# Optimization experiments

Hardware: AMD Instinct MI355X
Metric: run time of the kernel (lower is better)

## Reference

```python
import jax, jax.numpy as jnp
import numpy as np

N_G, E_G, E_H, E_I = 100000, 1000000, 1500000, 2000000
IN_FEATS = 64


def setup_inputs() -> dict:
    key = jax.random.key(0)
    ks = jax.random.split(key, 13)
    inp = {
        'z': jax.random.randint(ks[0], (N_G,), 0, 8),
        'src_g': jax.random.randint(ks[1], (E_G,), 0, N_G),
        'dst_g': jax.random.randint(ks[2], (E_G,), 0, N_G),
        'src_h': jax.random.randint(ks[3], (E_H,), 0, E_G),
        'dst_h': jax.random.randint(ks[4], (E_H,), 0, E_G),
        'src_i': jax.random.randint(ks[5], (E_I,), 0, E_H),
        'dst_i': jax.random.randint(ks[6], (E_I,), 0, E_H),
    }
    for n, k in zip(['e1', 'e2', 'e3', 'e4', 'e5', 'e6'], ks[7:13]):
        inp[n] = jax.random.normal(k, (2, IN_FEATS), dtype=jnp.float32)
    return inp


def reference(z, src_g, dst_g, src_h, dst_h, src_i, dst_i, e1, e2, e3, e4, e5, e6):
    # hop 1: g.apply_edges(send_z) -> per-edge endpoint labels, become h node data
    z_src = z[src_g]            # [E_G]
    z_dst = z[dst_g]            # [E_G]
    # hop 2: h.apply_edges(send_z2) -> become i node data
    z_src_src = z_src[src_h]    # [E_H]
    z_dst_dst = z_dst[dst_h]    # [E_H]
    # hop 3: i.apply_edges(comparison4) on edge endpoints of i
    za = z_src_src[src_i]       # [E_I]
    zb = z_src_src[dst_i]
    zc = z_dst_dst[src_i]
    zd = z_dst_dst[dst_i]
    zac = (za == zc).astype(jnp.int32)
    zab = (za == zb).astype(jnp.int32)
    zbc = (zc == zb).astype(jnp.int32)
    zad = (za == zd).astype(jnp.int32)
    zcd = (zc == zd).astype(jnp.int32)
    zbd = (zb == zd).astype(jnp.int32)
    # six 2-row embedding lookups summed -> [E_I, IN_FEATS]
    h = e1[zac] + e2[zab] + e3[zbc] + e4[zad] + e5[zcd] + e6[zbd]
    return h
```

## Files before the change

kernel.cpp:

```cpp
#include <hip/hip_runtime.h>


#define N_FEAT 64
#define WEPB   4096

typedef float f4 __attribute__((ext_vector_type(4)));

__global__ void hop1_table_kernel(const int* __restrict__ z,
                                  const int* __restrict__ src_g,
                                  const int* __restrict__ dst_g,
                                  unsigned short* __restrict__ zg,
                                  const float* __restrict__ e1,
                                  const float* __restrict__ e2,
                                  const float* __restrict__ e3,
                                  const float* __restrict__ e4,
                                  const float* __restrict__ e5,
                                  const float* __restrict__ e6,
                                  float* __restrict__ table,
                                  int n) {
    int i  = blockIdx.x * blockDim.x + threadIdx.x;
    int n8 = n >> 3;
    if (i < n8) {
        const int4* s4 = (const int4*)src_g;
        const int4* d4 = (const int4*)dst_g;
        int4 sa = s4[2 * i], sb = s4[2 * i + 1];
        int4 da = d4[2 * i], db = d4[2 * i + 1];
        unsigned r0 = ((unsigned)z[sa.x] & 0xffu) | (((unsigned)z[da.x] & 0xffu) << 8)
                    | (((unsigned)z[sa.y] & 0xffu) << 16) | (((unsigned)z[da.y] & 0xffu) << 24);
        unsigned r1 = ((unsigned)z[sa.z] & 0xffu) | (((unsigned)z[da.z] & 0xffu) << 8)
                    | (((unsigned)z[sa.w] & 0xffu) << 16) | (((unsigned)z[da.w] & 0xffu) << 24);
        unsigned r2 = ((unsigned)z[sb.x] & 0xffu) | (((unsigned)z[db.x] & 0xffu) << 8)
                    | (((unsigned)z[sb.y] & 0xffu) << 16) | (((unsigned)z[db.y] & 0xffu) << 24);
        unsigned r3 = ((unsigned)z[sb.z] & 0xffu) | (((unsigned)z[db.z] & 0xffu) << 8)
                    | (((unsigned)z[sb.w] & 0xffu) << 16) | (((unsigned)z[db.w] & 0xffu) << 24);
        ((uint4*)zg)[i] = make_uint4(r0, r1, r2, r3);
    } else {
        int e = (n8 << 3) + (i - n8);
        if (e < n) {
            zg[e] = (unsigned short)(((unsigned)z[src_g[e]] & 0xffu)
                                   | (((unsigned)z[dst_g[e]] & 0xffu) << 8));
        }
    }
    if (blockIdx.x < 16) {
        int idx = blockIdx.x * 256 + threadIdx.x;
        int cmb = idx >> 6;
        int f   = idx & (N_FEAT - 1);
        float v = e1[((cmb >> 0) & 1) * N_FEAT + f];
        v      += e2[((cmb >> 1) & 1) * N_FEAT + f];
        v      += e3[((cmb >> 2) & 1) * N_FEAT + f];
        v      += e4[((cmb >> 3) & 1) * N_FEAT + f];
        v      += e5[((cmb >> 4) & 1) * N_FEAT + f];
        v      += e6[((cmb >> 5) & 1) * N_FEAT + f];
        table[idx] = v;
    }
}

__global__ void hop2_kernel(const unsigned short* __restrict__ zg,
                            const int* __restrict__ src_h,
                            const int* __restrict__ dst_h,
                            unsigned short* __restrict__ zh,
                            int n) {
    int i  = blockIdx.x * blockDim.x + threadIdx.x;
    int n8 = n >> 3;
    if (i < n8) {
        const int4* s4 = (const int4*)src_h;
        const int4* d4 = (const int4*)dst_h;
        int4 sa = s4[2 * i], sb = s4[2 * i + 1];
        int4 da = d4[2 * i], db = d4[2 * i + 1];
        unsigned a0 = zg[sa.x], b0 = zg[da.x];
        unsigned a1 = zg[sa.y], b1 = zg[da.y];
        unsigned a2 = zg[sa.z], b2 = zg[da.z];
        unsigned a3 = zg[sa.w], b3 = zg[da.w];
        unsigned a4 = zg[sb.x], b4 = zg[db.x];
        unsigned a5 = zg[sb.y], b5 = zg[db.y];
        unsigned a6 = zg[sb.z], b6 = zg[db.z];
        unsigned a7 = zg[sb.w], b7 = zg[db.w];
        unsigned r0 = (a0 & 0xffu) | (b0 & 0xff00u) | ((a1 & 0xffu) << 16) | ((b1 & 0xff00u) << 16);
        unsigned r1 = (a2 & 0xffu) | (b2 & 0xff00u) | ((a3 & 0xffu) << 16) | ((b3 & 0xff00u) << 16);
        unsigned r2 = (a4 & 0xffu) | (b4 & 0xff00u) | ((a5 & 0xffu) << 16) | ((b5 & 0xff00u) << 16);
        unsigned r3 = (a6 & 0xffu) | (b6 & 0xff00u) | ((a7 & 0xffu) << 16) | ((b7 & 0xff00u) << 16);
        ((uint4*)zh)[i] = make_uint4(r0, r1, r2, r3);
    } else {
        int e = (n8 << 3) + (i - n8);
        if (e < n) {
            unsigned a = zg[src_h[e]], b = zg[dst_h[e]];
            zh[e] = (unsigned short)((a & 0xffu) | (b & 0xff00u));
        }
    }
}

__device__ __forceinline__ unsigned combo6(unsigned p, unsigned q) {
    unsigned za = p & 0xffu, zc = p >> 8;
    unsigned zb = q & 0xffu, zd = q >> 8;
    return (unsigned)(za == zc)
         | ((unsigned)(za == zb) << 1)
         | ((unsigned)(zc == zb) << 2)
         | ((unsigned)(za == zd) << 3)
         | ((unsigned)(zc == zd) << 4)
         | ((unsigned)(zb == zd) << 5);
}

__global__ __launch_bounds__(256)
void fused_k3_kernel(const unsigned short* __restrict__ zh,
                     const int* __restrict__ src_i,
                     const int* __restrict__ dst_i,
                     const float* __restrict__ table,
                     float* __restrict__ out,
                     int nEdges) {
    __shared__ f4   tbl[64 * 16];
    __shared__ uint4 cmbv[WEPB / 16];
    const int tid = threadIdx.x;
    const long long e0 = (long long)blockIdx.x * WEPB;
    int nb = nEdges - (int)e0; if (nb > WEPB) nb = WEPB;

    const f4* t4 = (const f4*)table;
#pragma unroll
    for (int k = 0; k < 4; ++k)
        tbl[k * 256 + tid] = t4[k * 256 + tid];

    if (nb == WEPB) {
        const int4* si = (const int4*)(src_i + e0);
        const int4* di = (const int4*)(dst_i + e0);
        int4 s0 = si[tid * 4 + 0], s1 = si[tid * 4 + 1],
             s2 = si[tid * 4 + 2], s3 = si[tid * 4 + 3];
        int4 d0 = di[tid * 4 + 0], d1 = di[tid * 4 + 1],
             d2 = di[tid * 4 + 2], d3 = di[tid * 4 + 3];
        unsigned r0 =  combo6(zh[s0.x], zh[d0.x])
                    | (combo6(zh[s0.y], zh[d0.y]) << 8)
                    | (combo6(zh[s0.z], zh[d0.z]) << 16)
                    | (combo6(zh[s0.w], zh[d0.w]) << 24);
        unsigned r1 =  combo6(zh[s1.x], zh[d1.x])
                    | (combo6(zh[s1.y], zh[d1.y]) << 8)
                    | (combo6(zh[s1.z], zh[d1.z]) << 16)
                    | (combo6(zh[s1.w], zh[d1.w]) << 24);
        unsigned r2 =  combo6(zh[s2.x], zh[d2.x])
                    | (combo6(zh[s2.y], zh[d2.y]) << 8)
                    | (combo6(zh[s2.z], zh[d2.z]) << 16)
                    | (combo6(zh[s2.w], zh[d2.w]) << 24);
        unsigned r3 =  combo6(zh[s3.x], zh[d3.x])
                    | (combo6(zh[s3.y], zh[d3.y]) << 8)
                    | (combo6(zh[s3.z], zh[d3.z]) << 16)
                    | (combo6(zh[s3.w], zh[d3.w]) << 24);
        cmbv[tid] = make_uint4(r0, r1, r2, r3);
    } else {
        unsigned r[4] = {0u, 0u, 0u, 0u};
        for (int j = 0; j < 16; ++j) {
            int le = tid * 16 + j;
            if (le < nb) {
                long long e = e0 + le;
                unsigned c = combo6(zh[src_i[e]], zh[dst_i[e]]);
                r[j >> 2] |= c << ((j & 3) * 8);
            }
        }
        cmbv[tid] = make_uint4(r[0], r[1], r[2], r[3]);
    }
    __syncthreads();

    const unsigned char* cmb = (const unsigned char*)cmbv;
    const int  w      = tid >> 6;
    const int  lane   = tid & 63;
    const int  c      = lane & 15;
    const int  leBase = w * (WEPB / 4) + (lane >> 4);
    const long long fBase = e0 * 16 + (long long)w * (WEPB * 16 / 4) + lane;
    constexpr int ITER = WEPB * 16 / 4 / 64;

    if (nb == WEPB) {
#pragma unroll 4
        for (int i = 0; i < ITER; ++i) {
            int le = leBase + i * 4;
            ((f4*)out)[fBase + (long long)i * 64] = tbl[(int)cmb[le] * 16 + c];
        }
    } else {
        const long long total = (long long)nEdges * 16;
#pragma unroll 4
        for (int i = 0; i < ITER; ++i) {
            long long f = fBase + (long long)i * 64;
            if (f < total) {
                int le = leBase + i * 4;
                ((f4*)out)[f] = tbl[(int)cmb[le] * 16 + c];
            }
        }
    }
}

extern "C" void kernel_launch(void* const* d_in, const int* in_sizes, int n_in,
                              void* d_out, int out_size, void* d_ws, size_t ws_size,
                              hipStream_t stream) {
    const int* z     = (const int*)d_in[0];
    const int* src_g = (const int*)d_in[1];
    const int* dst_g = (const int*)d_in[2];
    const int* src_h = (const int*)d_in[3];
    const int* dst_h = (const int*)d_in[4];
    const int* src_i = (const int*)d_in[5];
    const int* dst_i = (const int*)d_in[6];
    const float* e1  = (const float*)d_in[7];
    const float* e2  = (const float*)d_in[8];
    const float* e3  = (const float*)d_in[9];
    const float* e4  = (const float*)d_in[10];
    const float* e5  = (const float*)d_in[11];
    const float* e6  = (const float*)d_in[12];

    int E_G = in_sizes[1];
    int E_H = in_sizes[3];
    int E_I = in_sizes[5];

    char* ws = (char*)d_ws;
    float* table = (float*)ws;
    size_t off   = 64 * N_FEAT * sizeof(float);
    unsigned short* zg = (unsigned short*)(ws + off);
    off += (size_t)E_G * sizeof(unsigned short);
    off  = (off + 255) & ~(size_t)255;
    unsigned short* zh = (unsigned short*)(ws + off);

    float* out = (float*)d_out;

    {
        int n8 = E_G >> 3, nth = n8 + (E_G - (n8 << 3));
        int blocks = (nth + 255) / 256;
        if (blocks < 16) blocks = 16;
        hop1_table_kernel<<<blocks, 256, 0, stream>>>(z, src_g, dst_g, zg,
                                                      e1, e2, e3, e4, e5, e6,
                                                      table, E_G);
    }
    {
        int n8 = E_H >> 3, nth = n8 + (E_H - (n8 << 3));
        hop2_kernel<<<(nth + 255) / 256, 256, 0, stream>>>(zg, src_h, dst_h, zh, E_H);
    }
    {
        int blocks = (E_I + WEPB - 1) / WEPB;
        fused_k3_kernel<<<blocks, 256, 0, stream>>>(zh, src_i, dst_i, table, out, E_I);
    }
}
```

Measured before the change: 141.7 us.

## Fuse all three hops into one cooperative kernel with grid-wide syncs

Merges the hop-1/table kernel, the hop-2 kernel and the final gather/expand kernel into a single cooperative launch that separates the phases with grid.sync(). The aim is to remove the launch and drain gaps between the three dependent kernels. The per-block edge count of the last phase is halved so the grid, about 977 blocks, can be co-resident under __launch_bounds__(256,4), a requirement of cooperative launch. In exchange it adds two grid-wide barriers, whose cost on AMD GPUs can be several microseconds, and each of the first two phases gets only one pass with no grid-stride loop.

```diff
diff --git a/kernel.cpp b/kernel.cpp
--- a/kernel.cpp
+++ b/kernel.cpp
@@ -1,93 +1,13 @@
 #include <hip/hip_runtime.h>
+#include <hip/hip_cooperative_groups.h>
+
+namespace cg = cooperative_groups;
 
 
 #define N_FEAT 64
-#define WEPB   4096
+#define CWEPB  2048
 
 typedef float f4 __attribute__((ext_vector_type(4)));
-
-__global__ void hop1_table_kernel(const int* __restrict__ z,
-                                  const int* __restrict__ src_g,
-                                  const int* __restrict__ dst_g,
-                                  unsigned short* __restrict__ zg,
-                                  const float* __restrict__ e1,
-                                  const float* __restrict__ e2,
-                                  const float* __restrict__ e3,
-                                  const float* __restrict__ e4,
-                                  const float* __restrict__ e5,
-                                  const float* __restrict__ e6,
-                                  float* __restrict__ table,
-                                  int n) {
-    int i  = blockIdx.x * blockDim.x + threadIdx.x;
-    int n8 = n >> 3;
-    if (i < n8) {
-        const int4* s4 = (const int4*)src_g;
-        const int4* d4 = (const int4*)dst_g;
-        int4 sa = s4[2 * i], sb = s4[2 * i + 1];
-        int4 da = d4[2 * i], db = d4[2 * i + 1];
-        unsigned r0 = ((unsigned)z[sa.x] & 0xffu) | (((unsigned)z[da.x] & 0xffu) << 8)
-                    | (((unsigned)z[sa.y] & 0xffu) << 16) | (((unsigned)z[da.y] & 0xffu) << 24);
-        unsigned r1 = ((unsigned)z[sa.z] & 0xffu) | (((unsigned)z[da.z] & 0xffu) << 8)
-                    | (((unsigned)z[sa.w] & 0xffu) << 16) | (((unsigned)z[da.w] & 0xffu) << 24);
-        unsigned r2 = ((unsigned)z[sb.x] & 0xffu) | (((unsigned)z[db.x] & 0xffu) << 8)
-                    | (((unsigned)z[sb.y] & 0xffu) << 16) | (((unsigned)z[db.y] & 0xffu) << 24);
-        unsigned r3 = ((unsigned)z[sb.z] & 0xffu) | (((unsigned)z[db.z] & 0xffu) << 8)
-                    | (((unsigned)z[sb.w] & 0xffu) << 16) | (((unsigned)z[db.w] & 0xffu) << 24);
-        ((uint4*)zg)[i] = make_uint4(r0, r1, r2, r3);
-    } else {
-        int e = (n8 << 3) + (i - n8);
-        if (e < n) {
-            zg[e] = (unsigned short)(((unsigned)z[src_g[e]] & 0xffu)
-                                   | (((unsigned)z[dst_g[e]] & 0xffu) << 8));
-        }
-    }
-    if (blockIdx.x < 16) {
-        int idx = blockIdx.x * 256 + threadIdx.x;
-        int cmb = idx >> 6;
-        int f   = idx & (N_FEAT - 1);
-        float v = e1[((cmb >> 0) & 1) * N_FEAT + f];
-        v      += e2[((cmb >> 1) & 1) * N_FEAT + f];
-        v      += e3[((cmb >> 2) & 1) * N_FEAT + f];
-        v      += e4[((cmb >> 3) & 1) * N_FEAT + f];
-        v      += e5[((cmb >> 4) & 1) * N_FEAT + f];
-        v      += e6[((cmb >> 5) & 1) * N_FEAT + f];
-        table[idx] = v;
-    }
-}
-
-__global__ void hop2_kernel(const unsigned short* __restrict__ zg,
-                            const int* __restrict__ src_h,
-                            const int* __restrict__ dst_h,
-                            unsigned short* __restrict__ zh,
-                            int n) {
-    int i  = blockIdx.x * blockDim.x + threadIdx.x;
-    int n8 = n >> 3;
-    if (i < n8) {
-        const int4* s4 = (const int4*)src_h;
-        const int4* d4 = (const int4*)dst_h;
-        int4 sa = s4[2 * i], sb = s4[2 * i + 1];
-        int4 da = d4[2 * i], db = d4[2 * i + 1];
-        unsigned a0 = zg[sa.x], b0 = zg[da.x];
-        unsigned a1 = zg[sa.y], b1 = zg[da.y];
-        unsigned a2 = zg[sa.z], b2 = zg[da.z];
-        unsigned a3 = zg[sa.w], b3 = zg[da.w];
-        unsigned a4 = zg[sb.x], b4 = zg[db.x];
-        unsigned a5 = zg[sb.y], b5 = zg[db.y];
-        unsigned a6 = zg[sb.z], b6 = zg[db.z];
-        unsigned a7 = zg[sb.w], b7 = zg[db.w];
-        unsigned r0 = (a0 & 0xffu) | (b0 & 0xff00u) | ((a1 & 0xffu) << 16) | ((b1 & 0xff00u) << 16);
-        unsigned r1 = (a2 & 0xffu) | (b2 & 0xff00u) | ((a3 & 0xffu) << 16) | ((b3 & 0xff00u) << 16);
-        unsigned r2 = (a4 & 0xffu) | (b4 & 0xff00u) | ((a5 & 0xffu) << 16) | ((b5 & 0xff00u) << 16);
-        unsigned r3 = (a6 & 0xffu) | (b6 & 0xff00u) | ((a7 & 0xffu) << 16) | ((b7 & 0xff00u) << 16);
-        ((uint4*)zh)[i] = make_uint4(r0, r1, r2, r3);
-    } else {
-        int e = (n8 << 3) + (i - n8);
-        if (e < n) {
-            unsigned a = zg[src_h[e]], b = zg[dst_h[e]];
-            zh[e] = (unsigned short)((a & 0xffu) | (b & 0xff00u));
-        }
-    }
-}
 
 __device__ __forceinline__ unsigned combo6(unsigned p, unsigned q) {
     unsigned za = p & 0xffu, zc = p >> 8;
@@ -100,31 +20,113 @@
          | ((unsigned)(zb == zd) << 5);
 }
 
-__global__ __launch_bounds__(256)
-void fused_k3_kernel(const unsigned short* __restrict__ zh,
-                     const int* __restrict__ src_i,
-                     const int* __restrict__ dst_i,
-                     const float* __restrict__ table,
-                     float* __restrict__ out,
-                     int nEdges) {
-    __shared__ f4   tbl[64 * 16];
-    __shared__ uint4 cmbv[WEPB / 16];
-    const int tid = threadIdx.x;
-    const long long e0 = (long long)blockIdx.x * WEPB;
-    int nb = nEdges - (int)e0; if (nb > WEPB) nb = WEPB;
+__global__ __launch_bounds__(256, 4)
+void fused_all_kernel(const int* __restrict__ z,
+                      const int* __restrict__ src_g,
+                      const int* __restrict__ dst_g,
+                      const int* __restrict__ src_h,
+                      const int* __restrict__ dst_h,
+                      const int* __restrict__ src_i,
+                      const int* __restrict__ dst_i,
+                      const float* __restrict__ e1,
+                      const float* __restrict__ e2,
+                      const float* __restrict__ e3,
+                      const float* __restrict__ e4,
+                      const float* __restrict__ e5,
+                      const float* __restrict__ e6,
+                      float* __restrict__ table,
+                      unsigned short* __restrict__ zg,
+                      unsigned short* __restrict__ zh,
+                      float* __restrict__ out,
+                      int E_G, int E_H, int E_I) {
+    cg::grid_group grid = cg::this_grid();
+    __shared__ f4    tbl[64 * 16];
+    __shared__ uint2 cmbv[CWEPB / 8];
+    const int tid  = threadIdx.x;
+    const int gtid = blockIdx.x * 256 + tid;
+
+    if (blockIdx.x < 16) {
+        int idx = blockIdx.x * 256 + tid;
+        int cmb = idx >> 6;
+        int f   = idx & (N_FEAT - 1);
+        float v = e1[((cmb >> 0) & 1) * N_FEAT + f];
+        v      += e2[((cmb >> 1) & 1) * N_FEAT + f];
+        v      += e3[((cmb >> 2) & 1) * N_FEAT + f];
+        v      += e4[((cmb >> 3) & 1) * N_FEAT + f];
+        v      += e5[((cmb >> 4) & 1) * N_FEAT + f];
+        v      += e6[((cmb >> 5) & 1) * N_FEAT + f];
+        table[idx] = v;
+    }
+    {
+        int n8 = E_G >> 3;
+        if (gtid < n8) {
+            const int4* s4 = (const int4*)src_g;
+            const int4* d4 = (const int4*)dst_g;
+            int4 sa = s4[2 * gtid], sb = s4[2 * gtid + 1];
+            int4 da = d4[2 * gtid], db = d4[2 * gtid + 1];
+            unsigned r0 = ((unsigned)z[sa.x] & 0xffu) | (((unsigned)z[da.x] & 0xffu) << 8)
+                        | (((unsigned)z[sa.y] & 0xffu) << 16) | (((unsigned)z[da.y] & 0xffu) << 24);
+            unsigned r1 = ((unsigned)z[sa.z] & 0xffu) | (((unsigned)z[da.z] & 0xffu) << 8)
+                        | (((unsigned)z[sa.w] & 0xffu) << 16) | (((unsigned)z[da.w] & 0xffu) << 24);
+            unsigned r2 = ((unsigned)z[sb.x] & 0xffu) | (((unsigned)z[db.x] & 0xffu) << 8)
+                        | (((unsigned)z[sb.y] & 0xffu) << 16) | (((unsigned)z[db.y] & 0xffu) << 24);
+            unsigned r3 = ((unsigned)z[sb.z] & 0xffu) | (((unsigned)z[db.z] & 0xffu) << 8)
+                        | (((unsigned)z[sb.w] & 0xffu) << 16) | (((unsigned)z[db.w] & 0xffu) << 24);
+            ((uint4*)zg)[gtid] = make_uint4(r0, r1, r2, r3);
+        } else {
+            int e = (n8 << 3) + (gtid - n8);
+            if (e < E_G) {
+                zg[e] = (unsigned short)(((unsigned)z[src_g[e]] & 0xffu)
+                                       | (((unsigned)z[dst_g[e]] & 0xffu) << 8));
+            }
+        }
+    }
+    grid.sync();
+
+    {
+        int n8 = E_H >> 3;
+        if (gtid < n8) {
+            const int4* s4 = (const int4*)src_h;
+            const int4* d4 = (const int4*)dst_h;
+            int4 sa = s4[2 * gtid], sb = s4[2 * gtid + 1];
+            int4 da = d4[2 * gtid], db = d4[2 * gtid + 1];
+            unsigned a0 = zg[sa.x], b0 = zg[da.x];
+            unsigned a1 = zg[sa.y], b1 = zg[da.y];
+            unsigned a2 = zg[sa.z], b2 = zg[da.z];
+            unsigned a3 = zg[sa.w], b3 = zg[da.w];
+            unsigned a4 = zg[sb.x], b4 = zg[db.x];
+            unsigned a5 = zg[sb.y], b5 = zg[db.y];
+            unsigned a6 = zg[sb.z], b6 = zg[db.z];
+            unsigned a7 = zg[sb.w], b7 = zg[db.w];
+            unsigned r0 = (a0 & 0xffu) | (b0 & 0xff00u) | ((a1 & 0xffu) << 16) | ((b1 & 0xff00u) << 16);
+            unsigned r1 = (a2 & 0xffu) | (b2 & 0xff00u) | ((a3 & 0xffu) << 16) | ((b3 & 0xff00u) << 16);
+            unsigned r2 = (a4 & 0xffu) | (b4 & 0xff00u) | ((a5 & 0xffu) << 16) | ((b5 & 0xff00u) << 16);
+            unsigned r3 = (a6 & 0xffu) | (b6 & 0xff00u) | ((a7 & 0xffu) << 16) | ((b7 & 0xff00u) << 16);
+            ((uint4*)zh)[gtid] = make_uint4(r0, r1, r2, r3);
+        } else {
+            int e = (n8 << 3) + (gtid - n8);
+            if (e < E_H) {
+                unsigned a = zg[src_h[e]], b = zg[dst_h[e]];
+                zh[e] = (unsigned short)((a & 0xffu) | (b & 0xff00u));
+            }
+        }
+    }
+    grid.sync();
+
+    const long long e0 = (long long)blockIdx.x * CWEPB;
+    if (e0 >= E_I) return;
+    int nb = E_I - (int)e0; if (nb > CWEPB) nb = CWEPB;
 
     const f4* t4 = (const f4*)table;
 #pragma unroll
     for (int k = 0; k < 4; ++k)
         tbl[k * 256 + tid] = t4[k * 256 + tid];
 
-    if (nb == WEPB) {
+    if (nb == CWEPB) {
         const int4* si = (const int4*)(src_i + e0);
         const int4* di = (const int4*)(dst_i + e0);
-        int4 s0 = si[tid * 4 + 0], s1 = si[tid * 4 + 1],
-             s2 = si[tid * 4 + 2], s3 = si[tid * 4 + 3];
-        int4 d0 = di[tid * 4 + 0], d1 = di[tid * 4 + 1],
-             d2 = di[tid * 4 + 2], d3 = di[tid * 4 + 3];
+        int4 s0 = si[tid * 2], s1 = si[tid * 2 + 1];
+        int4 d0 = di[tid * 2], d1 = di[tid * 2 + 1];
         unsigned r0 =  combo6(zh[s0.x], zh[d0.x])
                     | (combo6(zh[s0.y], zh[d0.y]) << 8)
                     | (combo6(zh[s0.z], zh[d0.z]) << 16)
@@ -133,26 +135,17 @@
                     | (combo6(zh[s1.y], zh[d1.y]) << 8)
                     | (combo6(zh[s1.z], zh[d1.z]) << 16)
                     | (combo6(zh[s1.w], zh[d1.w]) << 24);
-        unsigned r2 =  combo6(zh[s2.x], zh[d2.x])
-                    | (combo6(zh[s2.y], zh[d2.y]) << 8)
-                    | (combo6(zh[s2.z], zh[d2.z]) << 16)
-                    | (combo6(zh[s2.w], zh[d2.w]) << 24);
-        unsigned r3 =  combo6(zh[s3.x], zh[d3.x])
-                    | (combo6(zh[s3.y], zh[d3.y]) << 8)
-                    | (combo6(zh[s3.z], zh[d3.z]) << 16)
-                    | (combo6(zh[s3.w], zh[d3.w]) << 24);
-        cmbv[tid] = make_uint4(r0, r1, r2, r3);
+        cmbv[tid] = make_uint2(r0, r1);
     } else {
-        unsigned r[4] = {0u, 0u, 0u, 0u};
-        for (int j = 0; j < 16; ++j) {
-            int le = tid * 16 + j;
+        unsigned r[2] = {0u, 0u};
+        for (int j = 0; j < 8; ++j) {
+            int le = tid * 8 + j;
             if (le < nb) {
                 long long e = e0 + le;
-                unsigned c = combo6(zh[src_i[e]], zh[dst_i[e]]);
-                r[j >> 2] |= c << ((j & 3) * 8);
-            }
-        }
-        cmbv[tid] = make_uint4(r[0], r[1], r[2], r[3]);
+                r[j >> 2] |= combo6(zh[src_i[e]], zh[dst_i[e]]) << ((j & 3) * 8);
+            }
+        }
+        cmbv[tid] = make_uint2(r[0], r[1]);
     }
     __syncthreads();
 
@@ -160,18 +153,18 @@
     const int  w      = tid >> 6;
     const int  lane   = tid & 63;
     const int  c      = lane & 15;
-    const int  leBase = w * (WEPB / 4) + (lane >> 4);
-    const long long fBase = e0 * 16 + (long long)w * (WEPB * 16 / 4) + lane;
-    constexpr int ITER = WEPB * 16 / 4 / 64;
-
-    if (nb == WEPB) {
+    const int  leBase = w * (CWEPB / 4) + (lane >> 4);
+    const long long fBase = e0 * 16 + (long long)w * (CWEPB * 16 / 4) + lane;
+    constexpr int ITER = CWEPB * 16 / 4 / 64;
+
+    if (nb == CWEPB) {
 #pragma unroll 4
         for (int i = 0; i < ITER; ++i) {
             int le = leBase + i * 4;
             ((f4*)out)[fBase + (long long)i * 64] = tbl[(int)cmb[le] * 16 + c];
         }
     } else {
-        const long long total = (long long)nEdges * 16;
+        const long long total = (long long)E_I * 16;
 #pragma unroll 4
         for (int i = 0; i < ITER; ++i) {
             long long f = fBase + (long long)i * 64;
@@ -214,20 +207,21 @@
 
     float* out = (float*)d_out;
 
-    {
-        int n8 = E_G >> 3, nth = n8 + (E_G - (n8 << 3));
-        int blocks = (nth + 255) / 256;
-        if (blocks < 16) blocks = 16;
-        hop1_table_kernel<<<blocks, 256, 0, stream>>>(z, src_g, dst_g, zg,
-                                                      e1, e2, e3, e4, e5, e6,
-                                                      table, E_G);
-    }
-    {
-        int n8 = E_H >> 3, nth = n8 + (E_H - (n8 << 3));
-        hop2_kernel<<<(nth + 255) / 256, 256, 0, stream>>>(zg, src_h, dst_h, zh, E_H);
-    }
-    {
-        int blocks = (E_I + WEPB - 1) / WEPB;
-        fused_k3_kernel<<<blocks, 256, 0, stream>>>(zh, src_i, dst_i, table, out, E_I);
-    }
+    int b3 = (E_I + CWEPB - 1) / CWEPB;
+    int n8g = E_G >> 3, b1 = (n8g + (E_G - (n8g << 3)) + 255) / 256;
+    int n8h = E_H >> 3, b2 = (n8h + (E_H - (n8h << 3)) + 255) / 256;
+    int G = b3;
+    if (b1 > G) G = b1;
+    if (b2 > G) G = b2;
+    if (G < 16) G = 16;
+
+    void* args[] = {
+        (void*)&z, (void*)&src_g, (void*)&dst_g,
+        (void*)&src_h, (void*)&dst_h, (void*)&src_i, (void*)&dst_i,
+        (void*)&e1, (void*)&e2, (void*)&e3, (void*)&e4, (void*)&e5, (void*)&e6,
+        (void*)&table, (void*)&zg, (void*)&zh, (void*)&out,
+        (void*)&E_G, (void*)&E_H, (void*)&E_I
+    };
+    hipLaunchCooperativeKernel((const void*)fused_all_kernel,
+                               dim3(G), dim3(256), args, 0, stream);
 }
```

Measured after the change: 386.6 us. 173% more time.
